# Kernel optimization log

Measured on AMD Instinct MI355X. Metric: run time of the kernel, lower is better.

Reference implementation:

```python
import jax, jax.numpy as jnp
import numpy as np

N_NODES = 100000


def gcn_conv(x, src, dst, norm, W, b, n_nodes):
    # PyG GCNConv: h = x @ W; out[i] = sum_{j->i} norm_ij * h[j]; out += b
    h = x @ W  # [N, F_out]
    msg = h[src] * norm[:, None]  # [E+N, F_out] gather + scale
    out = jax.ops.segment_sum(msg, dst, num_segments=n_nodes)
    return out + b


def setup_inputs() -> dict:
    key = jax.random.key(0)
    ks = jax.random.split(key, 5)
    n, e = N_NODES, 1600000
    d_in, d_h, d_out = 512, 128, 40
    x = jax.random.normal(ks[0], (n, d_in), dtype=jnp.float32)
    edge_index = jax.random.randint(ks[1], (2, e), 0, n, dtype=jnp.int64)
    # Glorot-ish scaled weights
    W1 = jax.random.normal(ks[2], (d_in, d_h), dtype=jnp.float32) * (1.0 / np.sqrt(d_in))
    b1 = jnp.zeros((d_h,), dtype=jnp.float32)
    W2 = jax.random.normal(ks[3], (d_h, d_out), dtype=jnp.float32) * (1.0 / np.sqrt(d_h))
    b2 = jnp.zeros((d_out,), dtype=jnp.float32)
    return {"x": x, "edge_index": edge_index, "W1": W1, "b1": b1, "W2": W2, "b2": b2}


def reference(x, edge_index, W1, b1, W2, b2):
    n = x.shape[0]
    # add self-loops (PyG default add_self_loops=True)
    loop = jnp.arange(n, dtype=edge_index.dtype)
    src = jnp.concatenate([edge_index[0], loop])
    dst = jnp.concatenate([edge_index[1], loop])
    # symmetric normalization: deg^-1/2[src] * deg^-1/2[dst]
    deg = jax.ops.segment_sum(jnp.ones_like(dst, dtype=x.dtype), dst, num_segments=n)
    dinv = jnp.where(deg > 0, jax.lax.rsqrt(jnp.maximum(deg, 1.0)), 0.0)
    norm = dinv[src] * dinv[dst]
    h = gcn_conv(x, src, dst, norm, W1, b1, n)
    h = jax.nn.relu(h)
    h = gcn_conv(h, src, dst, norm, W2, b2, n)
    return jax.nn.log_softmax(h, axis=1)
```

## Files before the change

kernel.cpp:

```cpp
#include <hip/hip_runtime.h>
#include <math.h>

#define SCAN_B 512
#define NBSHIFT 8
#define CHUNK 8192

typedef __attribute__((ext_vector_type(8))) short short8;
typedef __attribute__((ext_vector_type(4))) float v4f;

__device__ __forceinline__ unsigned short f2bf(float f) {
    unsigned int u = __float_as_uint(f);
    u += 0x7FFFu + ((u >> 16) & 1u);
    return (unsigned short)(u >> 16);
}
__device__ __forceinline__ unsigned int packbf(float a, float b) {
    return (unsigned int)f2bf(a) | ((unsigned int)f2bf(b) << 16);
}
__device__ __forceinline__ void bf8_to_f32(uint4 v, float* f) {
    f[0] = __uint_as_float(v.x << 16); f[1] = __uint_as_float(v.x & 0xFFFF0000u);
    f[2] = __uint_as_float(v.y << 16); f[3] = __uint_as_float(v.y & 0xFFFF0000u);
    f[4] = __uint_as_float(v.z << 16); f[5] = __uint_as_float(v.z & 0xFFFF0000u);
    f[6] = __uint_as_float(v.w << 16); f[7] = __uint_as_float(v.w & 0xFFFF0000u);
}

__global__ void count_deg_kernel(const int* __restrict__ dst, int E, int* __restrict__ counts) {
    int e = blockIdx.x * blockDim.x + threadIdx.x;
    if (e < E) atomicAdd(&counts[dst[e]], 1);
}

__global__ void scan1_kernel(const int* __restrict__ counts, int N,
                             int* __restrict__ partial, int* __restrict__ blockSums) {
    __shared__ int sm[SCAN_B];
    int tid = threadIdx.x;
    int i = blockIdx.x * SCAN_B + tid;
    int v = (i < N) ? counts[i] : 0;
    sm[tid] = v;
    __syncthreads();
    for (int off = 1; off < SCAN_B; off <<= 1) {
        int t = (tid >= off) ? sm[tid - off] : 0;
        __syncthreads();
        sm[tid] += t;
        __syncthreads();
    }
    if (i < N) partial[i] = sm[tid] - v;
    if (tid == SCAN_B - 1) blockSums[blockIdx.x] = sm[tid];
}

__global__ void scan2_kernel(int* __restrict__ blockSums, int nb) {
    __shared__ int sm[256];
    int tid = threadIdx.x;
    int v = (tid < nb) ? blockSums[tid] : 0;
    sm[tid] = v;
    __syncthreads();
    for (int off = 1; off < 256; off <<= 1) {
        int t = (tid >= off) ? sm[tid - off] : 0;
        __syncthreads();
        sm[tid] += t;
        __syncthreads();
    }
    if (tid < nb) blockSums[tid] = sm[tid] - v;
}

__global__ void scan3_kernel(const int* __restrict__ counts, int* __restrict__ offsets,
                             const int* __restrict__ blockSums, int N, int E,
                             int* __restrict__ cursor, float* __restrict__ dinv) {
    int i = blockIdx.x * SCAN_B + threadIdx.x;
    if (i < N) {
        int off = offsets[i] + blockSums[blockIdx.x];
        offsets[i] = off;
        cursor[i] = off;
        dinv[i] = rsqrtf((float)(counts[i] + 1));
    }
    if (i == 0 && blockIdx.x == 0) offsets[N] = E;
}

__global__ void binbase_kernel(const int* __restrict__ offsets, int* __restrict__ bin_base,
                               int* __restrict__ bin_cursor, int nbins, int N) {
    int b = blockIdx.x * 256 + threadIdx.x;
    if (b <= nbins) {
        int node = b << NBSHIFT;
        if (node > N) node = N;
        bin_base[b] = offsets[node];
        if (b < nbins) bin_cursor[b] = offsets[node];
    }
}

__global__ __launch_bounds__(256) void binpass_kernel(const int* __restrict__ src,
                                                      const int* __restrict__ dst, int E,
                                                      int* __restrict__ bin_cursor,
                                                      unsigned int* __restrict__ bpairs, int nbins) {
    __shared__ unsigned int pk[CHUNK];
    __shared__ unsigned short binOf[CHUNK];
    __shared__ int hist[512];
    __shared__ int scanned[512];
    __shared__ int rank[512];
    __shared__ int gbase[512];
    int tid = threadIdx.x;
    int base = blockIdx.x * CHUNK;
    int cnt = E - base; if (cnt > CHUNK) cnt = CHUNK;

    for (int i = tid; i < 512; i += 256) { hist[i] = 0; rank[i] = 0; }
    __syncthreads();
    for (int i = tid; i < cnt; i += 256) {
        int d = dst[base + i];
        atomicAdd(&hist[d >> NBSHIFT], 1);
    }
    __syncthreads();
    scanned[tid] = hist[tid]; scanned[tid + 256] = hist[tid + 256];
    __syncthreads();
    for (int off = 1; off < 512; off <<= 1) {
        int i0 = tid, i1 = tid + 256;
        int v0 = (i0 >= off) ? scanned[i0 - off] : 0;
        int v1 = (i1 >= off) ? scanned[i1 - off] : 0;
        __syncthreads();
        scanned[i0] += v0; scanned[i1] += v1;
        __syncthreads();
    }
    for (int i = tid; i < cnt; i += 256) {
        int d = dst[base + i];
        int s = src[base + i];
        int b = d >> NBSHIFT;
        unsigned int p = (unsigned int)s | ((unsigned int)(d & 255) << 17);
        int r = atomicAdd(&rank[b], 1);
        int pos = scanned[b] - hist[b] + r;
        pk[pos] = p;
        binOf[pos] = (unsigned short)b;
    }
    __syncthreads();
    for (int b = tid; b < nbins; b += 256)
        if (hist[b] > 0) gbase[b] = atomicAdd(&bin_cursor[b], hist[b]);
    __syncthreads();
    for (int i = tid; i < cnt; i += 256) {
        int b = binOf[i];
        int local = i - (scanned[b] - hist[b]);
        bpairs[gbase[b] + local] = pk[i];
    }
}

__global__ __launch_bounds__(256) void binscatter_kernel(const unsigned int* __restrict__ bpairs,
                                                         const int* __restrict__ bin_base,
                                                         int* __restrict__ cursor,
                                                         int* __restrict__ ssrc) {
    int b = blockIdx.x;
    int start = bin_base[b], end = bin_base[b + 1];
    int dhigh = b << NBSHIFT;
    for (int i = start + threadIdx.x; i < end; i += 256) {
        unsigned int p = bpairs[i];
        int s = (int)(p & 0x1FFFFu);
        int d = dhigh | (int)(p >> 17);
        int pos = atomicAdd(&cursor[d], 1);
        ssrc[pos] = s;
    }
}

__global__ void w1cast_kernel(const float* __restrict__ W1, unsigned short* __restrict__ W1t) {
    int idx = blockIdx.x * 256 + threadIdx.x;
    int k = idx >> 7, n = idx & 127;
    W1t[n * 512 + k] = f2bf(W1[idx]);
}

#define BM 64
#define BK 64

__global__ __launch_bounds__(256) void gemm1_mfma_kernel(const float* __restrict__ X,
                                                         const unsigned short* __restrict__ W1t,
                                                         unsigned short* __restrict__ H, int N) {
    __shared__ unsigned short As[BM * 64];
    __shared__ unsigned short Bs[128 * 64];
    int tid = threadIdx.x;
    int wave = tid >> 6, lane = tid & 63;
    int quad = lane >> 4, lr = lane & 15;
    int mBase = (wave & 1) * 32, nBase = (wave >> 1) * 64;
    int rowBase = blockIdx.x * BM;

    v4f zero4 = {0.f, 0.f, 0.f, 0.f};
    v4f acc[2][4];
    #pragma unroll
    for (int i = 0; i < 2; i++)
        #pragma unroll
        for (int j = 0; j < 4; j++) acc[i][j] = zero4;

    float4 pfA[4];
    uint4  pfB[4];

    #define LOAD_A(K0)                                                             \
        _Pragma("unroll")                                                          \
        for (int t = 0; t < 4; t++) {                                              \
            int idx = tid + t * 256;                                               \
            int r = idx >> 4, f4 = idx & 15;                                       \
            int gr = rowBase + r;                                                  \
            pfA[t] = (gr < N) ? *(const float4*)(X + (size_t)gr * 512 + (K0) + f4 * 4) \
                              : make_float4(0.f, 0.f, 0.f, 0.f);                   \
        }
    #define LOAD_B(K0)                                                             \
        _Pragma("unroll")                                                          \
        for (int t = 0; t < 4; t++) {                                              \
            int idx = tid + t * 256;                                               \
            int n = idx >> 3, c = idx & 7;                                         \
            pfB[t] = *(const uint4*)(W1t + (size_t)n * 512 + (K0) + c * 8);        \
        }

    LOAD_A(0); LOAD_B(0);

    for (int k0 = 0; k0 < 512; k0 += BK) {
        __syncthreads();
        #pragma unroll
        for (int t = 0; t < 4; t++) {
            int idx = tid + t * 256;
            int r = idx >> 4, f4 = idx & 15;
            int c = f4 >> 1, half = f4 & 1;
            ushort4 b;
            b.x = f2bf(pfA[t].x); b.y = f2bf(pfA[t].y);
            b.z = f2bf(pfA[t].z); b.w = f2bf(pfA[t].w);
            *(ushort4*)(&As[r * 64 + ((c ^ (r & 7)) << 3) + half * 4]) = b;
        }
        #pragma unroll
        for (int t = 0; t < 4; t++) {
            int idx = tid + t * 256;
            int n = idx >> 3, c = idx & 7;
            *(uint4*)(&Bs[n * 64 + ((c ^ (n & 7)) << 3)]) = pfB[t];
        }
        __syncthreads();
        if (k0 + BK < 512) { LOAD_A(k0 + BK); LOAD_B(k0 + BK); }
        #pragma unroll
        for (int kc = 0; kc < BK; kc += 32) {
            int cb = kc >> 3;
            short8 aF[2], bF[4];
            #pragma unroll
            for (int i = 0; i < 2; i++) {
                int m = mBase + i * 16 + lr;
                aF[i] = *(const short8*)(&As[m * 64 + (((cb + quad) ^ (m & 7)) << 3)]);
            }
            #pragma unroll
            for (int j = 0; j < 4; j++) {
                int n = nBase + j * 16 + lr;
                bF[j] = *(const short8*)(&Bs[n * 64 + (((cb + quad) ^ (n & 7)) << 3)]);
            }
            #pragma unroll
            for (int i = 0; i < 2; i++)
                #pragma unroll
                for (int j = 0; j < 4; j++)
                    acc[i][j] = __builtin_amdgcn_mfma_f32_16x16x32_bf16(aF[i], bF[j], acc[i][j], 0, 0, 0);
        }
    }
    __syncthreads();
    unsigned short* Cs = Bs;
    #pragma unroll
    for (int i = 0; i < 2; i++) {
        #pragma unroll
        for (int r = 0; r < 4; r++) {
            int m = mBase + i * 16 + quad * 4 + r;
            #pragma unroll
            for (int j = 0; j < 4; j++)
                Cs[m * 128 + nBase + j * 16 + lr] = f2bf(acc[i][j][r]);
        }
    }
    __syncthreads();
    #pragma unroll
    for (int t = 0; t < 4; t++) {
        int idx = tid + t * 256;
        int row = idx >> 4, c = idx & 15;
        int gr = rowBase + row;
        if (gr < N)
            *(uint4*)(H + (size_t)gr * 128 + c * 8) = *(const uint4*)(Cs + row * 128 + c * 8);
    }
    #undef LOAD_A
    #undef LOAD_B
}

__global__ __launch_bounds__(256) void agg1_kernel(const unsigned short* __restrict__ h1,
                                                   const int* __restrict__ offsets,
                                                   const int* __restrict__ ssrc,
                                                   const float* __restrict__ dinv,
                                                   const float* __restrict__ bias,
                                                   unsigned short* __restrict__ a1, int N) {
    int lane = threadIdx.x & 15;
    int node = (blockIdx.x << 4) + (threadIdx.x >> 4);
    if (node >= N) return;
    const uint4* h = (const uint4*)h1;
    float di = dinv[node];
    float acc[8], t[8];
    bf8_to_f32(h[(size_t)node * 16 + lane], t);
    #pragma unroll
    for (int i = 0; i < 8; i++) acc[i] = di * t[i];
    int e = offsets[node], e1 = offsets[node + 1];
    for (; e + 3 < e1; e += 4) {
        int sA = ssrc[e], sB = ssrc[e + 1], sC = ssrc[e + 2], sD = ssrc[e + 3];
        float wA = dinv[sA], wB = dinv[sB], wC = dinv[sC], wD = dinv[sD];
        uint4 vA = h[(size_t)sA * 16 + lane];
        uint4 vB = h[(size_t)sB * 16 + lane];
        uint4 vC = h[(size_t)sC * 16 + lane];
        uint4 vD = h[(size_t)sD * 16 + lane];
        float fA[8], fB[8], fC[8], fD[8];
        bf8_to_f32(vA, fA); bf8_to_f32(vB, fB); bf8_to_f32(vC, fC); bf8_to_f32(vD, fD);
        #pragma unroll
        for (int i = 0; i < 8; i++) {
            acc[i] = fmaf(wA, fA[i], acc[i]);
            acc[i] = fmaf(wB, fB[i], acc[i]);
            acc[i] = fmaf(wC, fC[i], acc[i]);
            acc[i] = fmaf(wD, fD[i], acc[i]);
        }
    }
    for (; e < e1; e++) {
        int s = ssrc[e];
        float w = dinv[s];
        float fs[8];
        bf8_to_f32(h[(size_t)s * 16 + lane], fs);
        #pragma unroll
        for (int i = 0; i < 8; i++) acc[i] = fmaf(w, fs[i], acc[i]);
    }
    float4 b0 = ((const float4*)bias)[lane * 2];
    float4 b1v = ((const float4*)bias)[lane * 2 + 1];
    float bb[8] = {b0.x, b0.y, b0.z, b0.w, b1v.x, b1v.y, b1v.z, b1v.w};
    float o[8];
    #pragma unroll
    for (int i = 0; i < 8; i++) o[i] = fmaxf(fmaf(di, acc[i], bb[i]), 0.f);
    uint4 pv;
    pv.x = packbf(o[0], o[1]); pv.y = packbf(o[2], o[3]);
    pv.z = packbf(o[4], o[5]); pv.w = packbf(o[6], o[7]);
    ((uint4*)a1)[(size_t)node * 16 + lane] = pv;
}

__global__ __launch_bounds__(256) void gemm2_kernel(const unsigned short* __restrict__ A,
                                                    const float* __restrict__ W,
                                                    float* __restrict__ H, int N) {
    __shared__ float As2[128][64];
    __shared__ float Ws[128 * 40];
    int tid = threadIdx.x;
    int rowBase = blockIdx.x * 64;

    #pragma unroll
    for (int l = 0; l < 4; l++) {
        int e = tid + l * 256;
        int r = e >> 4;
        int kk = (e & 15) << 3;
        int grow = rowBase + r;
        float f[8] = {0.f, 0.f, 0.f, 0.f, 0.f, 0.f, 0.f, 0.f};
        if (grow < N) {
            uint4 v = *(const uint4*)(A + (size_t)grow * 128 + kk);
            bf8_to_f32(v, f);
        }
        #pragma unroll
        for (int q = 0; q < 8; q++) As2[kk + q][r] = f[q];
    }
    #pragma unroll
    for (int l = 0; l < 5; l++) {
        int e = tid + l * 256;
        *(float4*)&Ws[e << 2] = *(const float4*)&W[e << 2];
    }
    __syncthreads();

    int tx = tid & 7;
    int ty = tid >> 3;
    float acc[2][5];
    #pragma unroll
    for (int r = 0; r < 2; r++)
        #pragma unroll
        for (int c = 0; c < 5; c++) acc[r][c] = 0.f;

    #pragma unroll 8
    for (int k = 0; k < 128; k++) {
        float a0 = As2[k][ty * 2];
        float a1v = As2[k][ty * 2 + 1];
        #pragma unroll
        for (int c = 0; c < 5; c++) {
            float w = Ws[k * 40 + tx * 5 + c];
            acc[0][c] = fmaf(a0, w, acc[0][c]);
            acc[1][c] = fmaf(a1v, w, acc[1][c]);
        }
    }
    #pragma unroll
    for (int r = 0; r < 2; r++) {
        int grow = rowBase + ty * 2 + r;
        if (grow < N) {
            #pragma unroll
            for (int c = 0; c < 5; c++) H[grow * 40 + tx * 5 + c] = acc[r][c];
        }
    }
}

__global__ __launch_bounds__(256) void agg2_kernel(const float* __restrict__ h2,
                                                   const int* __restrict__ offsets,
                                                   const int* __restrict__ ssrc,
                                                   const float* __restrict__ dinv,
                                                   const float* __restrict__ bias,
                                                   float* __restrict__ out, int N) {
    int node = blockIdx.x * 4 + (threadIdx.x >> 6);
    int lane = threadIdx.x & 63;
    if (node >= N) return;
    float di = dinv[node];
    bool act = lane < 40;
    float acc = 0.f;
    if (act) acc = di * h2[(size_t)node * 40 + lane];
    int e = offsets[node], e1 = offsets[node + 1];
    for (; e + 3 < e1; e += 4) {
        int sa = ssrc[e], sb = ssrc[e + 1], sc = ssrc[e + 2], sd = ssrc[e + 3];
        float wa = dinv[sa], wb = dinv[sb], wc = dinv[sc], wd = dinv[sd];
        if (act) {
            float ha = h2[(size_t)sa * 40 + lane];
            float hb = h2[(size_t)sb * 40 + lane];
            float hc = h2[(size_t)sc * 40 + lane];
            float hd = h2[(size_t)sd * 40 + lane];
            acc = fmaf(wa, ha, acc); acc = fmaf(wb, hb, acc);
            acc = fmaf(wc, hc, acc); acc = fmaf(wd, hd, acc);
        }
    }
    for (; e < e1; e++) {
        int s = ssrc[e];
        float w = dinv[s];
        if (act) acc = fmaf(w, h2[(size_t)s * 40 + lane], acc);
    }
    float v = act ? fmaf(di, acc, bias[lane]) : -INFINITY;
    float m = v;
    #pragma unroll
    for (int off = 32; off; off >>= 1) m = fmaxf(m, __shfl_xor(m, off, 64));
    float ex = act ? expf(v - m) : 0.f;
    float s = ex;
    #pragma unroll
    for (int off = 32; off; off >>= 1) s += __shfl_xor(s, off, 64);
    if (act) out[(size_t)node * 40 + lane] = v - m - logf(s);
}

extern "C" void kernel_launch(void* const* d_in, const int* in_sizes, int n_in,
                              void* d_out, int out_size, void* d_ws, size_t ws_size,
                              hipStream_t stream) {
    const float* x  = (const float*)d_in[0];
    const int*   ei = (const int*)d_in[1];
    const float* W1 = (const float*)d_in[2];
    const float* b1 = (const float*)d_in[3];
    const float* W2 = (const float*)d_in[4];
    const float* b2 = (const float*)d_in[5];
    float* out = (float*)d_out;

    int N = in_sizes[0] / 512;
    int E = in_sizes[1] / 2;
    const int* src = ei;
    const int* dst = ei + E;
    int nbins = (N + 255) >> NBSHIFT;

    char* ws = (char*)d_ws;
    size_t off = 0;
    auto alloc = [&](size_t bytes) -> void* {
        void* p = ws + off;
        off += (bytes + 255) & ~(size_t)255;
        return p;
    };
    int*   counts    = (int*)alloc((size_t)N * 4);
    int*   offsets   = (int*)alloc((size_t)(N + 1) * 4);
    int*   cursor    = (int*)alloc((size_t)N * 4);
    float* dinv      = (float*)alloc((size_t)N * 4);
    int nb = (N + SCAN_B - 1) / SCAN_B;
    int*   blockSums = (int*)alloc((size_t)nb * 4);
    int*   bin_base  = (int*)alloc((size_t)(nbins + 1) * 4);
    int*   bin_cur   = (int*)alloc((size_t)nbins * 4);
    int*   ssrc      = (int*)alloc((size_t)E * 4);
    unsigned short* W1t = (unsigned short*)alloc((size_t)128 * 512 * 2);
    unsigned short* h1  = (unsigned short*)alloc((size_t)N * 128 * 2);
    unsigned short* a1  = (unsigned short*)alloc((size_t)N * 128 * 2);
    float* h2        = (float*)alloc((size_t)N * 40 * 4);
    unsigned int* bpairs = (unsigned int*)h1;
    (void)ws_size; (void)n_in; (void)out_size;

    hipMemsetAsync(counts, 0, (size_t)N * 4, stream);
    count_deg_kernel<<<(E + 255) / 256, 256, 0, stream>>>(dst, E, counts);
    scan1_kernel<<<nb, SCAN_B, 0, stream>>>(counts, N, offsets, blockSums);
    scan2_kernel<<<1, 256, 0, stream>>>(blockSums, nb);
    scan3_kernel<<<nb, SCAN_B, 0, stream>>>(counts, offsets, blockSums, N, E, cursor, dinv);
    binbase_kernel<<<(nbins + 256) / 256, 256, 0, stream>>>(offsets, bin_base, bin_cur, nbins, N);
    binpass_kernel<<<(E + CHUNK - 1) / CHUNK, 256, 0, stream>>>(src, dst, E, bin_cur, bpairs, nbins);
    binscatter_kernel<<<nbins, 256, 0, stream>>>(bpairs, bin_base, cursor, ssrc);
    w1cast_kernel<<<256, 256, 0, stream>>>(W1, W1t);
    gemm1_mfma_kernel<<<(N + BM - 1) / BM, 256, 0, stream>>>(x, W1t, h1, N);
    agg1_kernel<<<(N + 15) / 16, 256, 0, stream>>>(h1, offsets, ssrc, dinv, b1, a1, N);
    gemm2_kernel<<<(N + 63) / 64, 256, 0, stream>>>(a1, W2, h2, N);
    agg2_kernel<<<(N + 3) / 4, 256, 0, stream>>>(h2, offsets, ssrc, dinv, b2, out, N);
}
```

Measured before the change: 660.1 us.

## Enlarge gemm1 row tile to 128 and pre-swizzle W1 into LDS layout

The first GEMM now uses a 128-row tile: each wave computes a 64x64 output block, which doubles how often each W1 tile loaded into shared memory is reused. W1 is cast to bf16 and stored already in the swizzled per-K-block shared-memory layout, so tile loads become straight contiguous copies. X loads become 32-byte per-thread chunks packed into one 128-bit LDS store, and the output staging buffer is XOR-swizzled to avoid bank conflicts. The cost is more accumulator registers, which may lower occupancy, and half as many blocks.

```diff
diff --git a/kernel.cpp b/kernel.cpp
--- a/kernel.cpp
+++ b/kernel.cpp
@@ -153,81 +153,78 @@
     }
 }
 
-__global__ void w1cast_kernel(const float* __restrict__ W1, unsigned short* __restrict__ W1t) {
+__global__ void w1cast_kernel(const float* __restrict__ W1, unsigned short* __restrict__ W1s) {
     int idx = blockIdx.x * 256 + threadIdx.x;
     int k = idx >> 7, n = idx & 127;
-    W1t[n * 512 + k] = f2bf(W1[idx]);
-}
-
-#define BM 64
-#define BK 64
+    int dstIdx = ((k >> 6) << 13) | (n << 6) | ((((k >> 3) & 7) ^ (n & 7)) << 3) | (k & 7);
+    W1s[dstIdx] = f2bf(W1[idx]);
+}
+
+#define BM1 128
+#define BK1 64
 
 __global__ __launch_bounds__(256) void gemm1_mfma_kernel(const float* __restrict__ X,
-                                                         const unsigned short* __restrict__ W1t,
+                                                         const unsigned short* __restrict__ W1s,
                                                          unsigned short* __restrict__ H, int N) {
-    __shared__ unsigned short As[BM * 64];
-    __shared__ unsigned short Bs[128 * 64];
+    __shared__ unsigned short SMEM[16384];
+    unsigned short* As = SMEM;
+    unsigned short* Bs = SMEM + 8192;
     int tid = threadIdx.x;
     int wave = tid >> 6, lane = tid & 63;
     int quad = lane >> 4, lr = lane & 15;
-    int mBase = (wave & 1) * 32, nBase = (wave >> 1) * 64;
-    int rowBase = blockIdx.x * BM;
+    int mBase = (wave & 1) * 64, nBase = (wave >> 1) * 64;
+    int rowBase = blockIdx.x * BM1;
 
     v4f zero4 = {0.f, 0.f, 0.f, 0.f};
-    v4f acc[2][4];
-    #pragma unroll
-    for (int i = 0; i < 2; i++)
+    v4f acc[4][4];
+    #pragma unroll
+    for (int i = 0; i < 4; i++)
         #pragma unroll
         for (int j = 0; j < 4; j++) acc[i][j] = zero4;
 
-    float4 pfA[4];
+    float4 pfA0[4], pfA1[4];
     uint4  pfB[4];
 
-    #define LOAD_A(K0)                                                             \
-        _Pragma("unroll")                                                          \
-        for (int t = 0; t < 4; t++) {                                              \
-            int idx = tid + t * 256;                                               \
-            int r = idx >> 4, f4 = idx & 15;                                       \
-            int gr = rowBase + r;                                                  \
-            pfA[t] = (gr < N) ? *(const float4*)(X + (size_t)gr * 512 + (K0) + f4 * 4) \
-                              : make_float4(0.f, 0.f, 0.f, 0.f);                   \
-        }
-    #define LOAD_B(K0)                                                             \
-        _Pragma("unroll")                                                          \
-        for (int t = 0; t < 4; t++) {                                              \
-            int idx = tid + t * 256;                                               \
-            int n = idx >> 3, c = idx & 7;                                         \
-            pfB[t] = *(const uint4*)(W1t + (size_t)n * 512 + (K0) + c * 8);        \
-        }
+    #define LOAD_A(K0)                                                                  \
+        _Pragma("unroll")                                                               \
+        for (int t = 0; t < 4; t++) {                                                   \
+            int idx = tid + t * 256;                                                    \
+            int r = idx >> 3, c = idx & 7;                                              \
+            int gr = rowBase + r;                                                       \
+            const float4* p = (const float4*)(X + (size_t)gr * 512 + (K0) + c * 8);     \
+            bool ok = gr < N;                                                           \
+            pfA0[t] = ok ? p[0] : make_float4(0.f, 0.f, 0.f, 0.f);                      \
+            pfA1[t] = ok ? p[1] : make_float4(0.f, 0.f, 0.f, 0.f);                      \
+        }
+    #define LOAD_B(K0)                                                                  \
+        _Pragma("unroll")                                                               \
+        for (int t = 0; t < 4; t++)                                                     \
+            pfB[t] = *(const uint4*)(W1s + (((K0) >> 6) << 13) + ((tid + t * 256) << 3));
 
     LOAD_A(0); LOAD_B(0);
 
-    for (int k0 = 0; k0 < 512; k0 += BK) {
+    for (int k0 = 0; k0 < 512; k0 += BK1) {
         __syncthreads();
         #pragma unroll
         for (int t = 0; t < 4; t++) {
             int idx = tid + t * 256;
-            int r = idx >> 4, f4 = idx & 15;
-            int c = f4 >> 1, half = f4 & 1;
-            ushort4 b;
-            b.x = f2bf(pfA[t].x); b.y = f2bf(pfA[t].y);
-            b.z = f2bf(pfA[t].z); b.w = f2bf(pfA[t].w);
-            *(ushort4*)(&As[r * 64 + ((c ^ (r & 7)) << 3) + half * 4]) = b;
-        }
-        #pragma unroll
-        for (int t = 0; t < 4; t++) {
-            int idx = tid + t * 256;
-            int n = idx >> 3, c = idx & 7;
-            *(uint4*)(&Bs[n * 64 + ((c ^ (n & 7)) << 3)]) = pfB[t];
-        }
-        __syncthreads();
-        if (k0 + BK < 512) { LOAD_A(k0 + BK); LOAD_B(k0 + BK); }
-        #pragma unroll
-        for (int kc = 0; kc < BK; kc += 32) {
+            int r = idx >> 3, c = idx & 7;
+            uint4 v;
+            v.x = packbf(pfA0[t].x, pfA0[t].y); v.y = packbf(pfA0[t].z, pfA0[t].w);
+            v.z = packbf(pfA1[t].x, pfA1[t].y); v.w = packbf(pfA1[t].z, pfA1[t].w);
+            *(uint4*)(&As[(r << 6) + ((c ^ (r & 7)) << 3)]) = v;
+        }
+        #pragma unroll
+        for (int t = 0; t < 4; t++)
+            *(uint4*)(&Bs[(tid + t * 256) << 3]) = pfB[t];
+        __syncthreads();
+        if (k0 + BK1 < 512) { LOAD_A(k0 + BK1); LOAD_B(k0 + BK1); }
+        #pragma unroll
+        for (int kc = 0; kc < BK1; kc += 32) {
             int cb = kc >> 3;
-            short8 aF[2], bF[4];
+            short8 aF[4], bF[4];
             #pragma unroll
-            for (int i = 0; i < 2; i++) {
+            for (int i = 0; i < 4; i++) {
                 int m = mBase + i * 16 + lr;
                 aF[i] = *(const short8*)(&As[m * 64 + (((cb + quad) ^ (m & 7)) << 3)]);
             }
@@ -237,32 +234,33 @@
                 bF[j] = *(const short8*)(&Bs[n * 64 + (((cb + quad) ^ (n & 7)) << 3)]);
             }
             #pragma unroll
-            for (int i = 0; i < 2; i++)
+            for (int i = 0; i < 4; i++)
                 #pragma unroll
                 for (int j = 0; j < 4; j++)
                     acc[i][j] = __builtin_amdgcn_mfma_f32_16x16x32_bf16(aF[i], bF[j], acc[i][j], 0, 0, 0);
         }
     }
     __syncthreads();
-    unsigned short* Cs = Bs;
-    #pragma unroll
-    for (int i = 0; i < 2; i++) {
+    unsigned short* Cs = SMEM;
+    #pragma unroll
+    for (int i = 0; i < 4; i++) {
         #pragma unroll
         for (int r = 0; r < 4; r++) {
             int m = mBase + i * 16 + quad * 4 + r;
             #pragma unroll
             for (int j = 0; j < 4; j++)
-                Cs[m * 128 + nBase + j * 16 + lr] = f2bf(acc[i][j][r]);
-        }
-    }
-    __syncthreads();
-    #pragma unroll
-    for (int t = 0; t < 4; t++) {
+                Cs[m * 128 + ((nBase + j * 16 + lr) ^ ((m & 7) << 4))] = f2bf(acc[i][j][r]);
+        }
+    }
+    __syncthreads();
+    #pragma unroll
+    for (int t = 0; t < 8; t++) {
         int idx = tid + t * 256;
         int row = idx >> 4, c = idx & 15;
         int gr = rowBase + row;
         if (gr < N)
-            *(uint4*)(H + (size_t)gr * 128 + c * 8) = *(const uint4*)(Cs + row * 128 + c * 8);
+            *(uint4*)(H + (size_t)gr * 128 + c * 8) =
+                *(const uint4*)(&Cs[row * 128 + ((c * 8) ^ ((row & 7) << 4))]);
     }
     #undef LOAD_A
     #undef LOAD_B
@@ -454,7 +452,7 @@
     int*   bin_base  = (int*)alloc((size_t)(nbins + 1) * 4);
     int*   bin_cur   = (int*)alloc((size_t)nbins * 4);
     int*   ssrc      = (int*)alloc((size_t)E * 4);
-    unsigned short* W1t = (unsigned short*)alloc((size_t)128 * 512 * 2);
+    unsigned short* W1s = (unsigned short*)alloc((size_t)128 * 512 * 2);
     unsigned short* h1  = (unsigned short*)alloc((size_t)N * 128 * 2);
     unsigned short* a1  = (unsigned short*)alloc((size_t)N * 128 * 2);
     float* h2        = (float*)alloc((size_t)N * 40 * 4);
@@ -469,8 +467,8 @@
     binbase_kernel<<<(nbins + 256) / 256, 256, 0, stream>>>(offsets, bin_base, bin_cur, nbins, N);
     binpass_kernel<<<(E + CHUNK - 1) / CHUNK, 256, 0, stream>>>(src, dst, E, bin_cur, bpairs, nbins);
     binscatter_kernel<<<nbins, 256, 0, stream>>>(bpairs, bin_base, cursor, ssrc);
-    w1cast_kernel<<<256, 256, 0, stream>>>(W1, W1t);
-    gemm1_mfma_kernel<<<(N + BM - 1) / BM, 256, 0, stream>>>(x, W1t, h1, N);
+    w1cast_kernel<<<256, 256, 0, stream>>>(W1, W1s);
+    gemm1_mfma_kernel<<<(N + BM1 - 1) / BM1, 256, 0, stream>>>(x, W1s, h1, N);
     agg1_kernel<<<(N + 15) / 16, 256, 0, stream>>>(h1, offsets, ssrc, dinv, b1, a1, N);
     gemm2_kernel<<<(N + 63) / 64, 256, 0, stream>>>(a1, W2, h2, N);
     agg2_kernel<<<(N + 3) / 4, 256, 0, stream>>>(h2, offsets, ssrc, dinv, b2, out, N);
```

After: 646.8 us. 2.0% less time.
